# Kernel tuning notes

Measured on AMD Instinct MI355X. Metric: run time of the kernel, lower is better.

Reference implementation:

```python
import jax, jax.numpy as jnp
import numpy as np

N = 8192
NODE_DIM = 512
HIDDEN = 256
N_CLASSES = 16
N_EDGES = 262144


def build_adj_mat(edge_index, n):
    # Dense {0,1} adjacency from COO edge list, plus self-loops so every
    # row of the masked softmax has at least one finite entry.
    adj = jnp.zeros((n, n), dtype=jnp.float32)
    adj = adj.at[edge_index[0], edge_index[1]].set(1.0)
    diag = jnp.arange(n)
    adj = adj.at[diag, diag].set(1.0)
    return adj


def setup_inputs() -> dict:
    key = jax.random.key(0)
    k_x, k_e, k_W, k_a1, k_a2, k_fw, k_fb = jax.random.split(key, 7)
    x = jax.random.normal(k_x, (N, NODE_DIM), dtype=jnp.float32)
    edge_index = jax.random.randint(k_e, (2, N_EDGES), 0, N, dtype=jnp.int64)
    # xavier_uniform-style inits
    def xavier(k, shape):
        fan_in, fan_out = shape[1], shape[0]
        lim = float(np.sqrt(6.0 / (fan_in + fan_out)))
        return jax.random.uniform(k, shape, jnp.float32, -lim, lim)
    W = xavier(k_W, (HIDDEN, NODE_DIM))
    a1 = xavier(k_a1, (HIDDEN, 1))
    a2 = xavier(k_a2, (HIDDEN, 1))
    fc_w = xavier(k_fw, (N_CLASSES, HIDDEN))
    fc_b = jnp.zeros((N_CLASSES,), dtype=jnp.float32)
    return {"x": x, "edge_index": edge_index, "W": W, "a1": a1, "a2": a2,
            "fc_w": fc_w, "fc_b": fc_b}


def reference(x, edge_index, W, a1, a2, fc_w, fc_b):
    adj = build_adj_mat(edge_index, x.shape[0])
    h = x @ W.T                                   # [N, H]
    f1 = (h @ a1)[:, 0]                           # [N]
    f2 = (h @ a2)[:, 0]                           # [N]
    e = jax.nn.leaky_relu(f1[:, None] + f2[None, :], negative_slope=0.01)
    e = e * adj
    e = jnp.where(e == 0, -jnp.inf, e)            # mask non-edges (and exact zeros, as in source)
    alpha = jax.nn.softmax(e, axis=1)             # [N, N]
    out = jax.nn.elu(alpha @ h)                   # [N, H]
    logits = out @ fc_w.T + fc_b                  # [N, n_classes]
    return logits
```

## Files before the change

kernel.cpp:

```cpp
#include <hip/hip_runtime.h>
#include <hip/hip_bf16.h>
#include <stdint.h>
#include <math.h>

#define N_NODES 8192
#define NDIM    512
#define HID     256
#define NCLS    16
#define NE      262144
#define MWR     256
#define CAP     256

static __device__ __forceinline__ ushort f2bf(float f) {
    uint32_t u = __float_as_uint(f);
    uint32_t r = (u + 0x7FFFu + ((u >> 16) & 1u)) >> 16;
    return (ushort)r;
}
static __device__ __forceinline__ float bf2f(ushort u) {
    return __uint_as_float(((uint32_t)u) << 16);
}

__global__ __launch_bounds__(256) void build_mask(const void* __restrict__ edges,
                                                  uint32_t* __restrict__ mask) {
    const long long* p64 = (const long long*)edges;
    long long probe = p64[threadIdx.x & 31];
    const int is32 = __any(probe < 0 || probe >= (long long)N_NODES);

    int idx = blockIdx.x * blockDim.x + threadIdx.x;
    if (idx < NE) {
        int src, dst;
        if (is32) {
            const int* p = (const int*)edges;
            src = p[idx]; dst = p[NE + idx];
        } else {
            src = (int)p64[idx]; dst = (int)p64[NE + idx];
        }
        atomicOr(&mask[src * MWR + (dst >> 5)], 1u << (dst & 31));
    } else {
        int d = idx - NE;
        if (d < N_NODES) atomicOr(&mask[d * MWR + (d >> 5)], 1u << (d & 31));
    }
}

__global__ __launch_bounds__(256) void gemm_h(const float* __restrict__ x,
                                              const float* __restrict__ W,
                                              const float* __restrict__ a1,
                                              const float* __restrict__ a2,
                                              ushort* __restrict__ hb,
                                              float* __restrict__ f1,
                                              float* __restrict__ f2) {
    __shared__ float xs[32][68];
    __shared__ float ws[32][68];
    const int tid  = threadIdx.x;
    const int row0 = blockIdx.y * 64;
    const int col0 = blockIdx.x * 64;
    const int lr = tid >> 3;
    const int lc = (tid & 7) << 2;
    const int tx = tid & 15;
    const int ty = tid >> 4;
    float acc[4][4] = {};
    const float* xp = x + (size_t)(row0 + lr) * NDIM + lc;
    const float* wp = W + (size_t)(col0 + lr) * NDIM + lc;

    for (int k0 = 0; k0 < NDIM; k0 += 32) {
        float4 xa = *(const float4*)(xp + k0);
        float4 xb = *(const float4*)(xp + k0 + 32 * NDIM);
        float4 wa = *(const float4*)(wp + k0);
        float4 wb = *(const float4*)(wp + k0 + 32 * NDIM);
        __syncthreads();
        xs[lc + 0][lr] = xa.x; xs[lc + 1][lr] = xa.y; xs[lc + 2][lr] = xa.z; xs[lc + 3][lr] = xa.w;
        xs[lc + 0][lr + 32] = xb.x; xs[lc + 1][lr + 32] = xb.y; xs[lc + 2][lr + 32] = xb.z; xs[lc + 3][lr + 32] = xb.w;
        ws[lc + 0][lr] = wa.x; ws[lc + 1][lr] = wa.y; ws[lc + 2][lr] = wa.z; ws[lc + 3][lr] = wa.w;
        ws[lc + 0][lr + 32] = wb.x; ws[lc + 1][lr + 32] = wb.y; ws[lc + 2][lr + 32] = wb.z; ws[lc + 3][lr + 32] = wb.w;
        __syncthreads();
        #pragma unroll
        for (int kk = 0; kk < 32; ++kk) {
            float4 a = *(const float4*)&xs[kk][ty << 2];
            float4 b = *(const float4*)&ws[kk][tx << 2];
            acc[0][0] += a.x * b.x; acc[0][1] += a.x * b.y; acc[0][2] += a.x * b.z; acc[0][3] += a.x * b.w;
            acc[1][0] += a.y * b.x; acc[1][1] += a.y * b.y; acc[1][2] += a.y * b.z; acc[1][3] += a.y * b.w;
            acc[2][0] += a.z * b.x; acc[2][1] += a.z * b.y; acc[2][2] += a.z * b.z; acc[2][3] += a.z * b.w;
            acc[3][0] += a.w * b.x; acc[3][1] += a.w * b.y; acc[3][2] += a.w * b.z; acc[3][3] += a.w * b.w;
        }
    }
    const float4 a1c = *(const float4*)&a1[col0 + (tx << 2)];
    const float4 a2c = *(const float4*)&a2[col0 + (tx << 2)];
    #pragma unroll
    for (int i = 0; i < 4; ++i) {
        const int r = row0 + (ty << 2) + i;
        ushort4 hv;
        hv.x = f2bf(acc[i][0]); hv.y = f2bf(acc[i][1]);
        hv.z = f2bf(acc[i][2]); hv.w = f2bf(acc[i][3]);
        *(ushort4*)&hb[(size_t)r * HID + col0 + (tx << 2)] = hv;
        float p1 = acc[i][0] * a1c.x + acc[i][1] * a1c.y + acc[i][2] * a1c.z + acc[i][3] * a1c.w;
        float p2 = acc[i][0] * a2c.x + acc[i][1] * a2c.y + acc[i][2] * a2c.z + acc[i][3] * a2c.w;
        #pragma unroll
        for (int msk = 8; msk; msk >>= 1) {
            p1 += __shfl_xor(p1, msk);
            p2 += __shfl_xor(p2, msk);
        }
        if (tx == 0) {
            atomicAdd(&f1[r], p1);
            atomicAdd(&f2[r], p2);
        }
    }
}

__global__ __launch_bounds__(256) void aggregate(const uint32_t* __restrict__ mask,
                                                 const ushort* __restrict__ hb,
                                                 const float* __restrict__ f1,
                                                 const float* __restrict__ f2,
                                                 const float* __restrict__ fc_w,
                                                 const float* __restrict__ fc_b,
                                                 float* __restrict__ out) {
    __shared__ int   sh_j[CAP];
    __shared__ float sh_v[CAP];
    __shared__ int   sh_cnt;
    __shared__ float red_m[4];
    __shared__ float red_s[4];
    __shared__ float sh_out[HID];
    __shared__ float sh_fc[256];

    const int row  = blockIdx.x;
    const int tid  = threadIdx.x;
    const int lane = tid & 63;
    const int wv   = tid >> 6;
    if (tid == 0) sh_cnt = 0;
    __syncthreads();

    const float fi = f1[row];
    uint32_t w = mask[(size_t)row * MWR + tid];
    float m = -INFINITY, s = 0.f;
    while (w) {
        int b = __ffs(w) - 1;
        w &= w - 1;
        int j = (tid << 5) + b;
        float z = fi + f2[j];
        float v = z > 0.f ? z : 0.01f * z;
        if (v != 0.f) {
            int slot = atomicAdd(&sh_cnt, 1);
            if (slot < CAP) { sh_j[slot] = j; sh_v[slot] = v; }
            if (v > m) { s = s * __expf(m - v) + 1.f; m = v; }
            else       { s += __expf(v - m); }
        }
    }
    float M = m;
    #pragma unroll
    for (int off = 32; off; off >>= 1) M = fmaxf(M, __shfl_xor(M, off));
    float S = (m == -INFINITY) ? 0.f : s * __expf(m - M);
    #pragma unroll
    for (int off = 32; off; off >>= 1) S += __shfl_xor(S, off);
    if (lane == 0) { red_m[wv] = M; red_s[wv] = S; }
    __syncthreads();
    float Mt = fmaxf(fmaxf(red_m[0], red_m[1]), fmaxf(red_m[2], red_m[3]));
    float St = 0.f;
    #pragma unroll
    for (int k = 0; k < 4; ++k)
        if (red_m[k] != -INFINITY) St += red_s[k] * __expf(red_m[k] - Mt);

    const int cnt = min(sh_cnt, CAP);
    const float inv = 1.f / St;
    for (int n = tid; n < cnt; n += 256) sh_v[n] = __expf(sh_v[n] - Mt) * inv;
    __syncthreads();

    float acc = 0.f;
    const ushort* hcol = hb + tid;
    int n = 0;
    for (; n + 4 <= cnt; n += 4) {
        int j0 = sh_j[n+0], j1 = sh_j[n+1], j2 = sh_j[n+2], j3 = sh_j[n+3];
        float v0 = sh_v[n+0], v1 = sh_v[n+1], v2 = sh_v[n+2], v3 = sh_v[n+3];
        float h0 = bf2f(hcol[(size_t)j0 * HID]);
        float h1 = bf2f(hcol[(size_t)j1 * HID]);
        float h2 = bf2f(hcol[(size_t)j2 * HID]);
        float h3 = bf2f(hcol[(size_t)j3 * HID]);
        acc += v0 * h0 + v1 * h1 + v2 * h2 + v3 * h3;
    }
    for (; n < cnt; ++n) acc += sh_v[n] * bf2f(hcol[(size_t)sh_j[n] * HID]);

    sh_out[tid] = acc > 0.f ? acc : expm1f(acc);
    __syncthreads();

    const int c   = tid >> 4;
    const int seg = tid & 15;
    float p = 0.f;
    #pragma unroll
    for (int u = 0; u < 16; ++u) {
        int t = seg * 16 + u;
        p += sh_out[t] * fc_w[c * HID + t];
    }
    sh_fc[tid] = p;
    __syncthreads();
    if (tid < NCLS) {
        float t = fc_b[tid];
        #pragma unroll
        for (int q = 0; q < 16; ++q) t += sh_fc[tid * 16 + q];
        out[(size_t)row * NCLS + tid] = t;
    }
}

extern "C" void kernel_launch(void* const* d_in, const int* in_sizes, int n_in,
                              void* d_out, int out_size, void* d_ws, size_t ws_size,
                              hipStream_t stream) {
    const float* x    = (const float*)d_in[0];
    const void*  ei   = d_in[1];
    const float* W    = (const float*)d_in[2];
    const float* a1   = (const float*)d_in[3];
    const float* a2   = (const float*)d_in[4];
    const float* fc_w = (const float*)d_in[5];
    const float* fc_b = (const float*)d_in[6];
    float* out = (float*)d_out;

    char* ws = (char*)d_ws;
    uint32_t* mask = (uint32_t*)ws;
    float*    f1   = (float*)(ws + 8388608);
    float*    f2   = (float*)(ws + 8388608 + 32768);
    ushort*   hb   = (ushort*)(ws + 8388608 + 65536);

    hipMemsetAsync(ws, 0, 8388608 + 65536, stream);
    const int total = NE + N_NODES;
    build_mask<<<(total + 255) / 256, 256, 0, stream>>>(ei, mask);
    gemm_h<<<dim3(HID / 64, N_NODES / 64), 256, 0, stream>>>(x, W, a1, a2, hb, f1, f2);
    aggregate<<<N_NODES, 256, 0, stream>>>(mask, hb, f1, f2, fc_w, fc_b, out);
}
```

Baseline: 160.4 us.

## Process one graph row per wavefront in aggregate instead of one per block

The aggregate kernel now assigns each row to a single 64-lane wave, so a block of four waves handles four rows. Block-wide barriers are replaced by wave-local LDS fences, and each lane gathers four bf16 hidden values per neighbor with one vector load. The FC projection now reduces with shuffles. The neighbor capacity drops to 128, which truncates rows with more neighbors than that; with about 32 average degree this is assumed safe but is not guaranteed.

```diff
diff --git a/kernel.cpp b/kernel.cpp
--- a/kernel.cpp
+++ b/kernel.cpp
@@ -9,7 +9,7 @@
 #define NCLS    16
 #define NE      262144
 #define MWR     256
-#define CAP     256
+#define CAP     128
 
 static __device__ __forceinline__ ushort f2bf(float f) {
     uint32_t u = __float_as_uint(f);
@@ -18,6 +18,9 @@
 }
 static __device__ __forceinline__ float bf2f(ushort u) {
     return __uint_as_float(((uint32_t)u) << 16);
+}
+static __device__ __forceinline__ void wave_lds_fence() {
+    asm volatile("s_waitcnt lgkmcnt(0)" ::: "memory");
 }
 
 __global__ __launch_bounds__(256) void build_mask(const void* __restrict__ edges,
@@ -113,35 +116,39 @@
                                                  const float* __restrict__ fc_w,
                                                  const float* __restrict__ fc_b,
                                                  float* __restrict__ out) {
-    __shared__ int   sh_j[CAP];
-    __shared__ float sh_v[CAP];
-    __shared__ int   sh_cnt;
-    __shared__ float red_m[4];
-    __shared__ float red_s[4];
-    __shared__ float sh_out[HID];
-    __shared__ float sh_fc[256];
-
-    const int row  = blockIdx.x;
-    const int tid  = threadIdx.x;
-    const int lane = tid & 63;
-    const int wv   = tid >> 6;
-    if (tid == 0) sh_cnt = 0;
-    __syncthreads();
+    __shared__ int   sh_j[4][CAP];
+    __shared__ float sh_v[4][CAP];
+    __shared__ float sh_o[4][HID];
+    __shared__ int   sh_cnt[4];
+
+    const int wv   = threadIdx.x >> 6;
+    const int lane = threadIdx.x & 63;
+    const int row  = blockIdx.x * 4 + wv;
+    int*   jl = sh_j[wv];
+    float* vl = sh_v[wv];
+    float* ol = sh_o[wv];
+
+    if (lane == 0) sh_cnt[wv] = 0;
 
     const float fi = f1[row];
-    uint32_t w = mask[(size_t)row * MWR + tid];
+    uint4 mw = *(const uint4*)&mask[(size_t)row * MWR + lane * 4];
+
     float m = -INFINITY, s = 0.f;
-    while (w) {
-        int b = __ffs(w) - 1;
-        w &= w - 1;
-        int j = (tid << 5) + b;
-        float z = fi + f2[j];
-        float v = z > 0.f ? z : 0.01f * z;
-        if (v != 0.f) {
-            int slot = atomicAdd(&sh_cnt, 1);
-            if (slot < CAP) { sh_j[slot] = j; sh_v[slot] = v; }
-            if (v > m) { s = s * __expf(m - v) + 1.f; m = v; }
-            else       { s += __expf(v - m); }
+    #pragma unroll
+    for (int wi = 0; wi < 4; ++wi) {
+        uint32_t w = (&mw.x)[wi];
+        while (w) {
+            int b = __ffs(w) - 1;
+            w &= w - 1;
+            int j = (lane * 4 + wi) * 32 + b;
+            float z = fi + f2[j];
+            float v = z > 0.f ? z : 0.01f * z;
+            if (v != 0.f) {
+                int slot = atomicAdd(&sh_cnt[wv], 1);
+                if (slot < CAP) { jl[slot] = j; vl[slot] = v; }
+                if (v > m) { s = s * __expf(m - v) + 1.f; m = v; }
+                else       { s += __expf(v - m); }
+            }
         }
     }
     float M = m;
@@ -150,52 +157,54 @@
     float S = (m == -INFINITY) ? 0.f : s * __expf(m - M);
     #pragma unroll
     for (int off = 32; off; off >>= 1) S += __shfl_xor(S, off);
-    if (lane == 0) { red_m[wv] = M; red_s[wv] = S; }
-    __syncthreads();
-    float Mt = fmaxf(fmaxf(red_m[0], red_m[1]), fmaxf(red_m[2], red_m[3]));
-    float St = 0.f;
-    #pragma unroll
-    for (int k = 0; k < 4; ++k)
-        if (red_m[k] != -INFINITY) St += red_s[k] * __expf(red_m[k] - Mt);
-
-    const int cnt = min(sh_cnt, CAP);
-    const float inv = 1.f / St;
-    for (int n = tid; n < cnt; n += 256) sh_v[n] = __expf(sh_v[n] - Mt) * inv;
-    __syncthreads();
-
-    float acc = 0.f;
-    const ushort* hcol = hb + tid;
+
+    const int cnt = min(sh_cnt[wv], CAP);
+    wave_lds_fence();
+
+    const float inv = 1.f / S;
+    for (int n = lane; n < cnt; n += 64) vl[n] = __expf(vl[n] - M) * inv;
+    wave_lds_fence();
+
+    float a0 = 0.f, a1v = 0.f, a2v = 0.f, a3 = 0.f;
+    const ushort* hcol = hb + lane * 4;
     int n = 0;
     for (; n + 4 <= cnt; n += 4) {
-        int j0 = sh_j[n+0], j1 = sh_j[n+1], j2 = sh_j[n+2], j3 = sh_j[n+3];
-        float v0 = sh_v[n+0], v1 = sh_v[n+1], v2 = sh_v[n+2], v3 = sh_v[n+3];
-        float h0 = bf2f(hcol[(size_t)j0 * HID]);
-        float h1 = bf2f(hcol[(size_t)j1 * HID]);
-        float h2 = bf2f(hcol[(size_t)j2 * HID]);
-        float h3 = bf2f(hcol[(size_t)j3 * HID]);
-        acc += v0 * h0 + v1 * h1 + v2 * h2 + v3 * h3;
-    }
-    for (; n < cnt; ++n) acc += sh_v[n] * bf2f(hcol[(size_t)sh_j[n] * HID]);
-
-    sh_out[tid] = acc > 0.f ? acc : expm1f(acc);
-    __syncthreads();
-
-    const int c   = tid >> 4;
-    const int seg = tid & 15;
+        #pragma unroll
+        for (int u = 0; u < 4; ++u) {
+            int j   = jl[n + u];
+            float v = vl[n + u];
+            ushort4 hv = *(const ushort4*)(hcol + (size_t)j * HID);
+            a0 += v * bf2f(hv.x); a1v += v * bf2f(hv.y);
+            a2v += v * bf2f(hv.z); a3 += v * bf2f(hv.w);
+        }
+    }
+    for (; n < cnt; ++n) {
+        int j   = jl[n];
+        float v = vl[n];
+        ushort4 hv = *(const ushort4*)(hcol + (size_t)j * HID);
+        a0 += v * bf2f(hv.x); a1v += v * bf2f(hv.y);
+        a2v += v * bf2f(hv.z); a3 += v * bf2f(hv.w);
+    }
+    float4 e;
+    e.x = a0  > 0.f ? a0  : expm1f(a0);
+    e.y = a1v > 0.f ? a1v : expm1f(a1v);
+    e.z = a2v > 0.f ? a2v : expm1f(a2v);
+    e.w = a3  > 0.f ? a3  : expm1f(a3);
+    *(float4*)&ol[lane * 4] = e;
+    wave_lds_fence();
+
+    const int c = lane >> 2;
+    const int q = lane & 3;
     float p = 0.f;
     #pragma unroll
-    for (int u = 0; u < 16; ++u) {
-        int t = seg * 16 + u;
-        p += sh_out[t] * fc_w[c * HID + t];
-    }
-    sh_fc[tid] = p;
-    __syncthreads();
-    if (tid < NCLS) {
-        float t = fc_b[tid];
-        #pragma unroll
-        for (int q = 0; q < 16; ++q) t += sh_fc[tid * 16 + q];
-        out[(size_t)row * NCLS + tid] = t;
-    }
+    for (int i = 0; i < 64; i += 4) {
+        float4 o = *(const float4*)&ol[q * 64 + i];
+        float4 w = *(const float4*)&fc_w[c * HID + q * 64 + i];
+        p += o.x * w.x + o.y * w.y + o.z * w.z + o.w * w.w;
+    }
+    p += __shfl_xor(p, 1);
+    p += __shfl_xor(p, 2);
+    if (q == 0) out[(size_t)row * NCLS + c] = p + fc_b[c];
 }
 
 extern "C" void kernel_launch(void* const* d_in, const int* in_sizes, int n_in,
@@ -220,5 +229,5 @@
     const int total = NE + N_NODES;
     build_mask<<<(total + 255) / 256, 256, 0, stream>>>(ei, mask);
     gemm_h<<<dim3(HID / 64, N_NODES / 64), 256, 0, stream>>>(x, W, a1, a2, hb, f1, f2);
-    aggregate<<<N_NODES, 256, 0, stream>>>(mask, hb, f1, f2, fc_w, fc_b, out);
-}
+    aggregate<<<N_NODES / 4, 256, 0, stream>>>(mask, hb, f1, f2, fc_w, fc_b, out);
+}
```

New measurement: 151.9 us. 1.06x faster.
